# Kernel tuning notes

Measured on AMD Instinct MI355X. Metric: run time of the kernel, lower is better.

The kernel has to match this reference:

```python
import jax, jax.numpy as jnp
import numpy as np

N_NODES = 50000
N_EDGES = 600000
CH = 128


def _mlp(h, w1, b1, w2, b2):
    # Linear -> ReLU -> Linear (weights stored [in, out])
    return jax.nn.relu(h @ w1 + b1) @ w2 + b2


def setup_inputs() -> dict:
    key = jax.random.key(0)
    ks = jax.random.split(key, 12)
    def lin(k, fan_in, fan_out):
        bound = 1.0 / np.sqrt(fan_in)
        kw, kb = jax.random.split(k)
        w = jax.random.uniform(kw, (fan_in, fan_out), jnp.float32, -bound, bound)
        b = jax.random.uniform(kb, (fan_out,), jnp.float32, -bound, bound)
        return w, b
    ew1, eb1 = lin(ks[0], 3 * CH, CH)
    ew2, eb2 = lin(ks[1], CH, CH)
    nw1, nb1 = lin(ks[2], 2 * CH, CH)
    nw2, nb2 = lin(ks[3], CH, CH)
    x = jax.random.normal(ks[4], (N_NODES, CH), jnp.float32)
    edge_attr = jax.random.normal(ks[5], (N_EDGES, CH), jnp.float32)
    edge_index = jax.random.randint(ks[6], (2, N_EDGES), 0, N_NODES, jnp.int64 if jax.config.read('jax_enable_x64') else jnp.int32)
    return {"x": x, "edge_index": edge_index, "edge_attr": edge_attr,
            "ew1": ew1, "eb1": eb1, "ew2": ew2, "eb2": eb2,
            "nw1": nw1, "nb1": nb1, "nw2": nw2, "nb2": nb2}


def reference(x, edge_index, edge_attr, ew1, eb1, ew2, eb2, nw1, nb1, nw2, nb2):
    row, col = edge_index[0], edge_index[1]
    n = x.shape[0]
    # edge model: concat(source, target, edge_attr) -> MLP -> new edge_attr
    e_in = jnp.concatenate([x[row], x[col], edge_attr], axis=1)  # [E, 3*ch]
    new_edge_attr = _mlp(e_in, ew1, eb1, ew2, eb2)               # [E, ch]
    # node model: concat(x[col], new_edge_attr) -> MLP -> scatter_mean over row
    n_in = jnp.concatenate([x[col], new_edge_attr], axis=1)      # [E, 2*ch]
    msg = _mlp(n_in, nw1, nb1, nw2, nb2)                         # [E, ch]
    seg_sum = jax.ops.segment_sum(msg, row, num_segments=n)      # [N, ch]
    cnt = jax.ops.segment_sum(jnp.ones((msg.shape[0],), msg.dtype), row, num_segments=n)
    new_x = seg_sum / jnp.maximum(cnt, 1.0)[:, None]             # scatter_mean
    return new_x, new_edge_attr
```

## Files before the change

### kernel.cpp

```cpp
#include <hip/hip_runtime.h>
#include <stdint.h>

#define NN 50000
#define NE 600000
#define CH 128
#define RT 2
#define EPB 128

typedef __attribute__((ext_vector_type(8))) short short8;
typedef __attribute__((ext_vector_type(4))) float f32x4;
typedef __attribute__((ext_vector_type(4))) uint32_t u32x4;

__device__ __forceinline__ ushort f2bf(float f) {
  union { float f; uint32_t u; } v; v.f = f;
  uint32_t u = v.u;
  return (ushort)((u + 0x7FFFu + ((u >> 16) & 1u)) >> 16);
}
__device__ __forceinline__ float bf2f(uint32_t u16) {
  union { uint32_t u; float f; } t; t.u = u16 << 16; return t.f;
}
__device__ __forceinline__ uint32_t cvtpk_bf16(float a, float b) {
  uint32_t r;
  asm("v_cvt_pk_bf16_f32 %0, %1, %2" : "=v"(r) : "v"(a), "v"(b));
  return r;
}

__global__ void prep_frag_k(const float* __restrict__ ew1, const float* __restrict__ ew2,
                            const float* __restrict__ nw1, const float* __restrict__ nw2,
                            ushort* __restrict__ wB) {
  int idx = blockIdx.x * 256 + threadIdx.x;
  if (idx >= 114688) return;
  const float* src; int local;
  if (idx < 49152)      { src = ew1; local = idx; }
  else if (idx < 65536) { src = ew2; local = idx - 49152; }
  else if (idx < 98304) { src = nw1; local = idx - 65536; }
  else                  { src = nw2; local = idx - 98304; }
  int ks   = local >> 12;
  int rem  = local & 4095;
  int nt   = rem >> 9;
  int t    = rem & 511;
  int lane = t >> 3, i = t & 7;
  int k = ks * 32 + (lane >> 4) * 8 + i;
  int n = nt * 16 + (lane & 15);
  wB[idx] = f2bf(src[k * 128 + n]);
}

__global__ void convert_x_k(const float* __restrict__ x, ushort* __restrict__ xb) {
  int i = blockIdx.x * 256 + threadIdx.x;
  if (i >= NN * CH / 4) return;
  const float4 f = reinterpret_cast<const float4*>(x)[i];
  ushort4 r;
  r.x = f2bf(f.x); r.y = f2bf(f.y); r.z = f2bf(f.z); r.w = f2bf(f.w);
  reinterpret_cast<ushort4*>(xb)[i] = r;
}

__global__ void rank_k(const int* __restrict__ ei, unsigned* __restrict__ cnt,
                       unsigned* __restrict__ rank) {
  int e = blockIdx.x * 256 + threadIdx.x;
  if (e < NE) rank[e] = atomicAdd(&cnt[ei[e]], 1u);
}

__global__ void scan_k(const unsigned* __restrict__ cnt, unsigned* __restrict__ start) {
  __shared__ unsigned s[1024];
  const int CHUNK = (NN + 1023) / 1024;
  int t = threadIdx.x;
  int lo = t * CHUNK, hi = lo + CHUNK < NN ? lo + CHUNK : NN;
  unsigned sum = 0;
  for (int i = lo; i < hi; ++i) sum += cnt[i];
  s[t] = sum;
  __syncthreads();
  for (int off = 1; off < 1024; off <<= 1) {
    unsigned v = (t >= off) ? s[t - off] : 0u;
    __syncthreads();
    s[t] += v;
    __syncthreads();
  }
  unsigned run = t ? s[t - 1] : 0u;
  for (int i = lo; i < hi; ++i) { start[i] = run; run += cnt[i]; }
}

__global__ void dest_k(const int* __restrict__ ei, const unsigned* __restrict__ start,
                       const unsigned* __restrict__ rank, unsigned* __restrict__ dest) {
  int e = blockIdx.x * 256 + threadIdx.x;
  if (e < NE) dest[e] = start[ei[e]] + rank[e];
}

__device__ __forceinline__ void mm8(const ushort* Bcbuf, int lane,
                                    const short8 a[RT], f32x4 acc[RT][8]) {
#pragma unroll
  for (int nt = 0; nt < 8; ++nt) {
    short8 b = *reinterpret_cast<const short8*>(Bcbuf + nt * 512 + lane * 8);
#pragma unroll
    for (int rt = 0; rt < RT; ++rt)
      acc[rt][nt] = __builtin_amdgcn_mfma_f32_16x16x32_bf16(a[rt], b, acc[rt][nt], 0, 0, 0);
  }
}

__global__ __launch_bounds__(256, 3) void fused_k(
    const int* __restrict__ ei, const float* __restrict__ edge_attr,
    const ushort* __restrict__ wB,
    const float* __restrict__ eb1, const float* __restrict__ eb2,
    const float* __restrict__ nb1, const float* __restrict__ nb2,
    const ushort* __restrict__ xb, const unsigned* __restrict__ dest,
    ushort* __restrict__ msg, float* __restrict__ out_e)
{
  __shared__ ushort hbuf[4][RT * 16][136];
  __shared__ ushort Bc[2][4096];
  const int tid  = threadIdx.x;
  const int lane = tid & 63;
  const int widx = tid >> 6;
  const int wbase = blockIdx.x * EPB + widx * (RT * 16);
  const int l15 = lane & 15;
  const int g = lane >> 4;
  const int kg = g * 8;
  ushort (*h)[136] = hbuf[widx];

  const ushort* wsrc = wB + (size_t)tid * 16;
  short8 bt0, bt1;

#define LDB(ph) do { \
    bt0 = *reinterpret_cast<const short8*>(wsrc + (ph) * 4096); \
    bt1 = *reinterpret_cast<const short8*>(wsrc + (ph) * 4096 + 8); \
  } while (0)
#define STB(ph) do { \
    ushort* _d = &Bc[(ph) & 1][tid * 16]; \
    *reinterpret_cast<short8*>(_d) = bt0; \
    *reinterpret_cast<short8*>(_d + 8) = bt1; \
    __syncthreads(); \
  } while (0)

  int rowA[RT], colA[RT], eAc[RT];
#pragma unroll
  for (int rt = 0; rt < RT; ++rt) {
    int e = wbase + rt * 16 + l15;
    eAc[rt] = e < NE ? e : NE - 1;
    rowA[rt] = ei[eAc[rt]];
    colA[rt] = ei[NE + eAc[rt]];
  }

  const f32x4 zero4 = {0.f, 0.f, 0.f, 0.f};
  f32x4 acc[RT][8];

#pragma unroll
  for (int rt = 0; rt < RT; ++rt)
#pragma unroll
    for (int nt = 0; nt < 8; ++nt) acc[rt][nt] = zero4;

  LDB(0);
  short8 axr[4][RT], axc[4][RT];
#pragma unroll
  for (int ksl = 0; ksl < 4; ++ksl)
#pragma unroll
    for (int rt = 0; rt < RT; ++rt)
      axr[ksl][rt] = *reinterpret_cast<const short8*>(xb + rowA[rt] * CH + ksl * 32 + kg);
#pragma unroll
  for (int ksl = 0; ksl < 4; ++ksl)
#pragma unroll
    for (int rt = 0; rt < RT; ++rt)
      axc[ksl][rt] = *reinterpret_cast<const short8*>(xb + colA[rt] * CH + ksl * 32 + kg);
  STB(0);

#pragma unroll
  for (int p = 0; p < 4; ++p) {
    LDB(p + 1);
    mm8(Bc[p & 1], lane, axr[p], acc);
    STB(p + 1);
  }
#pragma unroll
  for (int p = 4; p < 8; ++p) {
    LDB(p + 1);
    mm8(Bc[p & 1], lane, axc[p - 4], acc);
    STB(p + 1);
  }
  float4 eaf[4][RT][2];
#pragma unroll
  for (int ksl = 0; ksl < 4; ++ksl)
#pragma unroll
    for (int rt = 0; rt < RT; ++rt) {
      const float* pp = edge_attr + (size_t)eAc[rt] * CH + ksl * 32 + kg;
      eaf[ksl][rt][0] = *reinterpret_cast<const float4*>(pp);
      eaf[ksl][rt][1] = *reinterpret_cast<const float4*>(pp + 4);
    }
#pragma unroll
  for (int p = 8; p < 12; ++p) {
    LDB(p + 1);
    short8 a[RT];
#pragma unroll
    for (int rt = 0; rt < RT; ++rt) {
      float4 f0 = eaf[p - 8][rt][0], f1 = eaf[p - 8][rt][1];
      union { u32x4 u; short8 s; } cv;
      cv.u = (u32x4){ cvtpk_bf16(f0.x, f0.y), cvtpk_bf16(f0.z, f0.w),
                      cvtpk_bf16(f1.x, f1.y), cvtpk_bf16(f1.z, f1.w) };
      a[rt] = cv.s;
    }
    mm8(Bc[p & 1], lane, a, acc);
    STB(p + 1);
  }
#pragma unroll
  for (int nt = 0; nt < 8; ++nt) {
    float bb = eb1[nt * 16 + l15];
#pragma unroll
    for (int rt = 0; rt < RT; ++rt)
#pragma unroll
      for (int r = 0; r < 4; r += 2) {
        float v0 = fmaxf(acc[rt][nt][r] + bb, 0.f);
        float v1 = fmaxf(acc[rt][nt][r + 1] + bb, 0.f);
        uint32_t pk = cvtpk_bf16(v0, v1);
        h[rt * 16 + g * 4 + r][nt * 16 + l15]     = (ushort)(pk & 0xffffu);
        h[rt * 16 + g * 4 + r + 1][nt * 16 + l15] = (ushort)(pk >> 16);
      }
  }

#pragma unroll
  for (int rt = 0; rt < RT; ++rt)
#pragma unroll
    for (int nt = 0; nt < 8; ++nt) acc[rt][nt] = zero4;
#pragma unroll
  for (int p = 12; p < 16; ++p) {
    LDB(p + 1);
    short8 a[RT];
#pragma unroll
    for (int rt = 0; rt < RT; ++rt)
      a[rt] = *reinterpret_cast<const short8*>(&h[rt * 16 + l15][(p - 12) * 32 + kg]);
    mm8(Bc[p & 1], lane, a, acc);
    STB(p + 1);
  }
  short8 axc2[4][RT];
#pragma unroll
  for (int ksl = 0; ksl < 4; ++ksl)
#pragma unroll
    for (int rt = 0; rt < RT; ++rt)
      axc2[ksl][rt] = *reinterpret_cast<const short8*>(xb + colA[rt] * CH + ksl * 32 + kg);
#pragma unroll
  for (int nt = 0; nt < 8; ++nt) {
    float bb = eb2[nt * 16 + l15];
#pragma unroll
    for (int rt = 0; rt < RT; ++rt) {
      float v[4];
#pragma unroll
      for (int r = 0; r < 4; ++r) {
        v[r] = acc[rt][nt][r] + bb;
        int erow = wbase + rt * 16 + g * 4 + r;
        if (erow < NE) out_e[(size_t)erow * CH + nt * 16 + l15] = v[r];
      }
#pragma unroll
      for (int r = 0; r < 4; r += 2) {
        uint32_t pk = cvtpk_bf16(v[r], v[r + 1]);
        h[rt * 16 + g * 4 + r][nt * 16 + l15]     = (ushort)(pk & 0xffffu);
        h[rt * 16 + g * 4 + r + 1][nt * 16 + l15] = (ushort)(pk >> 16);
      }
    }
  }

#pragma unroll
  for (int rt = 0; rt < RT; ++rt)
#pragma unroll
    for (int nt = 0; nt < 8; ++nt) acc[rt][nt] = zero4;
#pragma unroll
  for (int p = 16; p < 20; ++p) {
    LDB(p + 1);
    mm8(Bc[p & 1], lane, axc2[p - 16], acc);
    STB(p + 1);
  }
#pragma unroll
  for (int p = 20; p < 24; ++p) {
    LDB(p + 1);
    short8 a[RT];
#pragma unroll
    for (int rt = 0; rt < RT; ++rt)
      a[rt] = *reinterpret_cast<const short8*>(&h[rt * 16 + l15][(p - 20) * 32 + kg]);
    mm8(Bc[p & 1], lane, a, acc);
    STB(p + 1);
  }
#pragma unroll
  for (int nt = 0; nt < 8; ++nt) {
    float bb = nb1[nt * 16 + l15];
#pragma unroll
    for (int rt = 0; rt < RT; ++rt)
#pragma unroll
      for (int r = 0; r < 4; r += 2) {
        float v0 = fmaxf(acc[rt][nt][r] + bb, 0.f);
        float v1 = fmaxf(acc[rt][nt][r + 1] + bb, 0.f);
        uint32_t pk = cvtpk_bf16(v0, v1);
        h[rt * 16 + g * 4 + r][nt * 16 + l15]     = (ushort)(pk & 0xffffu);
        h[rt * 16 + g * 4 + r + 1][nt * 16 + l15] = (ushort)(pk >> 16);
      }
  }

#pragma unroll
  for (int rt = 0; rt < RT; ++rt)
#pragma unroll
    for (int nt = 0; nt < 8; ++nt) acc[rt][nt] = zero4;
#pragma unroll
  for (int p = 24; p < 27; ++p) {
    LDB(p + 1);
    short8 a[RT];
#pragma unroll
    for (int rt = 0; rt < RT; ++rt)
      a[rt] = *reinterpret_cast<const short8*>(&h[rt * 16 + l15][(p - 24) * 32 + kg]);
    mm8(Bc[p & 1], lane, a, acc);
    STB(p + 1);
  }
  {
    short8 a[RT];
#pragma unroll
    for (int rt = 0; rt < RT; ++rt)
      a[rt] = *reinterpret_cast<const short8*>(&h[rt * 16 + l15][3 * 32 + kg]);
    mm8(Bc[1], lane, a, acc);
  }
#pragma unroll
  for (int nt = 0; nt < 8; ++nt) {
    float bb = nb2[nt * 16 + l15];
#pragma unroll
    for (int rt = 0; rt < RT; ++rt)
#pragma unroll
      for (int r = 0; r < 4; r += 2) {
        uint32_t pk = cvtpk_bf16(acc[rt][nt][r] + bb, acc[rt][nt][r + 1] + bb);
        h[rt * 16 + g * 4 + r][nt * 16 + l15]     = (ushort)(pk & 0xffffu);
        h[rt * 16 + g * 4 + r + 1][nt * 16 + l15] = (ushort)(pk >> 16);
      }
  }
#pragma unroll
  for (int it = 0; it < RT * 4; ++it) {
    int row = it * 4 + g;
    int er = wbase + row;
    int col = l15 * 8;
    short8 v = *reinterpret_cast<const short8*>(&h[row][col]);
    if (er < NE) {
      unsigned dp = dest[er];
      *reinterpret_cast<short8*>(msg + (size_t)dp * CH + col) = v;
    }
  }
#undef LDB
#undef STB
}

__global__ __launch_bounds__(256) void reduce_k(const ushort* __restrict__ msg,
    const unsigned* __restrict__ cnt, const unsigned* __restrict__ start,
    float* __restrict__ out_x) {
  int w = blockIdx.x * 4 + (threadIdx.x >> 6);
  if (w >= NN) return;
  int lane = threadIdx.x & 63;
  unsigned deg = cnt[w], s = start[w];
  float a0 = 0.f, a1 = 0.f;
#pragma unroll 4
  for (unsigned j = 0; j < deg; ++j) {
    uint32_t pk = *reinterpret_cast<const uint32_t*>(msg + (size_t)(s + j) * CH + lane * 2);
    a0 += bf2f(pk & 0xffffu);
    a1 += bf2f(pk >> 16);
  }
  float inv = 1.0f / fmaxf((float)deg, 1.0f);
  float2 o; o.x = a0 * inv; o.y = a1 * inv;
  *reinterpret_cast<float2*>(out_x + (size_t)w * CH + lane * 2) = o;
}

extern "C" void kernel_launch(void* const* d_in, const int* in_sizes, int n_in,
                              void* d_out, int out_size, void* d_ws, size_t ws_size,
                              hipStream_t stream) {
  const float* x   = (const float*)d_in[0];
  const int*   ei  = (const int*)d_in[1];
  const float* ea  = (const float*)d_in[2];
  const float* ew1 = (const float*)d_in[3];
  const float* eb1 = (const float*)d_in[4];
  const float* ew2 = (const float*)d_in[5];
  const float* eb2 = (const float*)d_in[6];
  const float* nw1 = (const float*)d_in[7];
  const float* nb1 = (const float*)d_in[8];
  const float* nw2 = (const float*)d_in[9];
  const float* nb2 = (const float*)d_in[10];

  float* out_x = (float*)d_out;
  float* out_e = (float*)d_out + (size_t)NN * CH;

  char* wsb = (char*)d_ws;
  ushort*   msg    = (ushort*)wsb;
  ushort*   wB     = (ushort*)(wsb + 153600000);
  ushort*   xb     = (ushort*)(wsb + 153829376);
  unsigned* cnt    = (unsigned*)(wsb + 166629376);
  unsigned* start  = (unsigned*)(wsb + 166829376);
  unsigned* rank   = (unsigned*)(wsb + 167029376);
  unsigned* dest   = (unsigned*)(wsb + 169429376);

  hipMemsetAsync(cnt, 0, (size_t)NN * sizeof(unsigned), stream);

  prep_frag_k<<<448, 256, 0, stream>>>(ew1, ew2, nw1, nw2, wB);
  convert_x_k<<<(NN * CH / 4 + 255) / 256, 256, 0, stream>>>(x, xb);
  rank_k<<<(NE + 255) / 256, 256, 0, stream>>>(ei, cnt, rank);
  scan_k<<<1, 1024, 0, stream>>>(cnt, start);
  dest_k<<<(NE + 255) / 256, 256, 0, stream>>>(ei, start, rank, dest);

  int nblk = (NE + EPB - 1) / EPB;
  fused_k<<<nblk, 256, 0, stream>>>(ei, ea, wB, eb1, eb2, nb1, nb2, xb, dest, msg, out_e);

  reduce_k<<<(NN + 3) / 4, 256, 0, stream>>>(msg, cnt, start, out_x);
}
```

Baseline: 449.1 us.

## Use 1024-thread blocks sharing weight tiles and stream gathers just-in-time

The fused edge/node kernel now runs 16 waves per block instead of 4, so each staged weight tile in LDS is reused by four times as many edges. Each thread copies a smaller slice of the tile. The upfront gathers of x rows, x cols and edge_attr, which were held in many registers, are replaced by double-buffered per-phase prefetches. This should lower register pressure and the weight-load traffic per edge. The cost is larger per-block LDS (16 h buffers), heavier __syncthreads across 1024 threads, and less latency hiding, since each load is issued only one phase ahead.

```diff
diff --git a/kernel.cpp b/kernel.cpp
--- a/kernel.cpp
+++ b/kernel.cpp
@@ -5,7 +5,8 @@
 #define NE 600000
 #define CH 128
 #define RT 2
-#define EPB 128
+#define WAVES 16
+#define EPB (WAVES * 32)
 
 typedef __attribute__((ext_vector_type(8))) short short8;
 typedef __attribute__((ext_vector_type(4))) float f32x4;
@@ -96,7 +97,7 @@
   }
 }
 
-__global__ __launch_bounds__(256, 3) void fused_k(
+__global__ __launch_bounds__(1024, 1) void fused_k(
     const int* __restrict__ ei, const float* __restrict__ edge_attr,
     const ushort* __restrict__ wB,
     const float* __restrict__ eb1, const float* __restrict__ eb2,
@@ -104,7 +105,7 @@
     const ushort* __restrict__ xb, const unsigned* __restrict__ dest,
     ushort* __restrict__ msg, float* __restrict__ out_e)
 {
-  __shared__ ushort hbuf[4][RT * 16][136];
+  __shared__ ushort hbuf[WAVES][RT * 16][136];
   __shared__ ushort Bc[2][4096];
   const int tid  = threadIdx.x;
   const int lane = tid & 63;
@@ -115,17 +116,10 @@
   const int kg = g * 8;
   ushort (*h)[136] = hbuf[widx];
 
-  const ushort* wsrc = wB + (size_t)tid * 16;
-  short8 bt0, bt1;
-
-#define LDB(ph) do { \
-    bt0 = *reinterpret_cast<const short8*>(wsrc + (ph) * 4096); \
-    bt1 = *reinterpret_cast<const short8*>(wsrc + (ph) * 4096 + 8); \
-  } while (0)
+  ushort4 bt;
+#define LDB(ph) do { bt = *reinterpret_cast<const ushort4*>(wB + (size_t)(ph) * 4096 + tid * 4); } while (0)
 #define STB(ph) do { \
-    ushort* _d = &Bc[(ph) & 1][tid * 16]; \
-    *reinterpret_cast<short8*>(_d) = bt0; \
-    *reinterpret_cast<short8*>(_d + 8) = bt1; \
+    *reinterpret_cast<ushort4*>(&Bc[(ph) & 1][tid * 4]) = bt; \
     __syncthreads(); \
   } while (0)
 
@@ -146,48 +140,52 @@
 #pragma unroll
     for (int nt = 0; nt < 8; ++nt) acc[rt][nt] = zero4;
 
+  short8 ax[2][RT];
+  float4 ea2[2][RT][2];
+
   LDB(0);
-  short8 axr[4][RT], axc[4][RT];
-#pragma unroll
-  for (int ksl = 0; ksl < 4; ++ksl)
-#pragma unroll
-    for (int rt = 0; rt < RT; ++rt)
-      axr[ksl][rt] = *reinterpret_cast<const short8*>(xb + rowA[rt] * CH + ksl * 32 + kg);
-#pragma unroll
-  for (int ksl = 0; ksl < 4; ++ksl)
-#pragma unroll
-    for (int rt = 0; rt < RT; ++rt)
-      axc[ksl][rt] = *reinterpret_cast<const short8*>(xb + colA[rt] * CH + ksl * 32 + kg);
+#pragma unroll
+  for (int rt = 0; rt < RT; ++rt)
+    ax[0][rt] = *reinterpret_cast<const short8*>(xb + rowA[rt] * CH + kg);
   STB(0);
 
 #pragma unroll
-  for (int p = 0; p < 4; ++p) {
-    LDB(p + 1);
-    mm8(Bc[p & 1], lane, axr[p], acc);
-    STB(p + 1);
-  }
-#pragma unroll
-  for (int p = 4; p < 8; ++p) {
-    LDB(p + 1);
-    mm8(Bc[p & 1], lane, axc[p - 4], acc);
-    STB(p + 1);
-  }
-  float4 eaf[4][RT][2];
-#pragma unroll
-  for (int ksl = 0; ksl < 4; ++ksl)
+  for (int p = 0; p < 8; ++p) {
+    LDB(p + 1);
+    if (p + 1 < 4) {
+#pragma unroll
+      for (int rt = 0; rt < RT; ++rt)
+        ax[(p + 1) & 1][rt] = *reinterpret_cast<const short8*>(xb + rowA[rt] * CH + (p + 1) * 32 + kg);
+    } else if (p + 1 < 8) {
+#pragma unroll
+      for (int rt = 0; rt < RT; ++rt)
+        ax[(p + 1) & 1][rt] = *reinterpret_cast<const short8*>(xb + colA[rt] * CH + (p + 1 - 4) * 32 + kg);
+    } else {
+#pragma unroll
+      for (int rt = 0; rt < RT; ++rt) {
+        const float* pp = edge_attr + (size_t)eAc[rt] * CH + kg;
+        ea2[0][rt][0] = *reinterpret_cast<const float4*>(pp);
+        ea2[0][rt][1] = *reinterpret_cast<const float4*>(pp + 4);
+      }
+    }
+    mm8(Bc[p & 1], lane, ax[p & 1], acc);
+    STB(p + 1);
+  }
+#pragma unroll
+  for (int p = 8; p < 12; ++p) {
+    LDB(p + 1);
+    if (p < 11) {
+#pragma unroll
+      for (int rt = 0; rt < RT; ++rt) {
+        const float* pp = edge_attr + (size_t)eAc[rt] * CH + (p - 7) * 32 + kg;
+        ea2[(p + 1) & 1][rt][0] = *reinterpret_cast<const float4*>(pp);
+        ea2[(p + 1) & 1][rt][1] = *reinterpret_cast<const float4*>(pp + 4);
+      }
+    }
+    short8 a[RT];
 #pragma unroll
     for (int rt = 0; rt < RT; ++rt) {
-      const float* pp = edge_attr + (size_t)eAc[rt] * CH + ksl * 32 + kg;
-      eaf[ksl][rt][0] = *reinterpret_cast<const float4*>(pp);
-      eaf[ksl][rt][1] = *reinterpret_cast<const float4*>(pp + 4);
-    }
-#pragma unroll
-  for (int p = 8; p < 12; ++p) {
-    LDB(p + 1);
-    short8 a[RT];
-#pragma unroll
-    for (int rt = 0; rt < RT; ++rt) {
-      float4 f0 = eaf[p - 8][rt][0], f1 = eaf[p - 8][rt][1];
+      float4 f0 = ea2[p & 1][rt][0], f1 = ea2[p & 1][rt][1];
       union { u32x4 u; short8 s; } cv;
       cv.u = (u32x4){ cvtpk_bf16(f0.x, f0.y), cvtpk_bf16(f0.z, f0.w),
                       cvtpk_bf16(f1.x, f1.y), cvtpk_bf16(f1.z, f1.w) };
@@ -211,6 +209,7 @@
       }
   }
 
+  short8 axc2[4][RT];
 #pragma unroll
   for (int rt = 0; rt < RT; ++rt)
 #pragma unroll
@@ -218,6 +217,9 @@
 #pragma unroll
   for (int p = 12; p < 16; ++p) {
     LDB(p + 1);
+#pragma unroll
+    for (int rt = 0; rt < RT; ++rt)
+      axc2[p - 12][rt] = *reinterpret_cast<const short8*>(xb + colA[rt] * CH + (p - 12) * 32 + kg);
     short8 a[RT];
 #pragma unroll
     for (int rt = 0; rt < RT; ++rt)
@@ -225,12 +227,6 @@
     mm8(Bc[p & 1], lane, a, acc);
     STB(p + 1);
   }
-  short8 axc2[4][RT];
-#pragma unroll
-  for (int ksl = 0; ksl < 4; ++ksl)
-#pragma unroll
-    for (int rt = 0; rt < RT; ++rt)
-      axc2[ksl][rt] = *reinterpret_cast<const short8*>(xb + colA[rt] * CH + ksl * 32 + kg);
 #pragma unroll
   for (int nt = 0; nt < 8; ++nt) {
     float bb = eb2[nt * 16 + l15];
@@ -390,7 +386,7 @@
   dest_k<<<(NE + 255) / 256, 256, 0, stream>>>(ei, start, rank, dest);
 
   int nblk = (NE + EPB - 1) / EPB;
-  fused_k<<<nblk, 256, 0, stream>>>(ei, ea, wB, eb1, eb2, nb1, nb2, xb, dest, msg, out_e);
+  fused_k<<<nblk, 1024, 0, stream>>>(ei, ea, wB, eb1, eb2, nb1, nb2, xb, dest, msg, out_e);
 
   reduce_k<<<(NN + 3) / 4, 256, 0, stream>>>(msg, cnt, start, out_x);
 }
```

After: 580.0 us. 29.2% more time.

## Stage weight slices two at a time with quad LDS buffer and fewer barriers

Applied to the files above, without the earlier changes.

Restructures the weight-streaming pipeline so each barrier covers two 32-wide K slices, using a 4-slot LDS ring and two register sets of prefetched weight data. Barrier count drops by about half. Other changes: the second x[col] gather is removed by reusing axc, edge_attr is converted to bf16 at load time, dest indices are prefetched early, and MFMA blocks run at raised wave priority. It costs more registers and LDS, and occupancy is lowered from 3 to 2 blocks per CU.

```diff
diff --git a/kernel.cpp b/kernel.cpp
--- a/kernel.cpp
+++ b/kernel.cpp
@@ -96,7 +96,7 @@
   }
 }
 
-__global__ __launch_bounds__(256, 3) void fused_k(
+__global__ __launch_bounds__(256, 2) void fused_k(
     const int* __restrict__ ei, const float* __restrict__ edge_attr,
     const ushort* __restrict__ wB,
     const float* __restrict__ eb1, const float* __restrict__ eb2,
@@ -105,7 +105,7 @@
     ushort* __restrict__ msg, float* __restrict__ out_e)
 {
   __shared__ ushort hbuf[4][RT * 16][136];
-  __shared__ ushort Bc[2][4096];
+  __shared__ ushort Bc[4][4096];
   const int tid  = threadIdx.x;
   const int lane = tid & 63;
   const int widx = tid >> 6;
@@ -115,19 +115,40 @@
   const int kg = g * 8;
   ushort (*h)[136] = hbuf[widx];
 
-  const ushort* wsrc = wB + (size_t)tid * 16;
-  short8 bt0, bt1;
-
-#define LDB(ph) do { \
-    bt0 = *reinterpret_cast<const short8*>(wsrc + (ph) * 4096); \
-    bt1 = *reinterpret_cast<const short8*>(wsrc + (ph) * 4096 + 8); \
+  short8 bt[2][4];
+
+#define LDB2(set, ph) do { \
+    const ushort* _s = wB + (size_t)(ph) * 4096 + tid * 16; \
+    bt[set][0] = *reinterpret_cast<const short8*>(_s); \
+    bt[set][1] = *reinterpret_cast<const short8*>(_s + 8); \
+    bt[set][2] = *reinterpret_cast<const short8*>(_s + 4096); \
+    bt[set][3] = *reinterpret_cast<const short8*>(_s + 4096 + 8); \
   } while (0)
-#define STB(ph) do { \
-    ushort* _d = &Bc[(ph) & 1][tid * 16]; \
-    *reinterpret_cast<short8*>(_d) = bt0; \
-    *reinterpret_cast<short8*>(_d + 8) = bt1; \
+#define STB2(set, ph) do { \
+    ushort* _d0 = &Bc[(ph) & 3][tid * 16]; \
+    ushort* _d1 = &Bc[((ph) + 1) & 3][tid * 16]; \
+    *reinterpret_cast<short8*>(_d0)     = bt[set][0]; \
+    *reinterpret_cast<short8*>(_d0 + 8) = bt[set][1]; \
+    *reinterpret_cast<short8*>(_d1)     = bt[set][2]; \
+    *reinterpret_cast<short8*>(_d1 + 8) = bt[set][3]; \
+  } while (0)
+#define STEP(s, A0, A1, DO_LDB, DO_STB) do { \
     __syncthreads(); \
+    __builtin_amdgcn_s_setprio(1); \
+    mm8(Bc[(2 * (s)) & 3], lane, A0, acc); \
+    mm8(Bc[(2 * (s) + 1) & 3], lane, A1, acc); \
+    __builtin_amdgcn_s_setprio(0); \
+    if (DO_LDB) LDB2((s) & 1, 2 * (s) + 4); \
+    if (DO_STB) STB2(((s) + 1) & 1, 2 * (s) + 2); \
   } while (0)
+#define LDH(dst, ksl) do { \
+    _Pragma("unroll") \
+    for (int _rt = 0; _rt < RT; ++_rt) \
+      dst[_rt] = *reinterpret_cast<const short8*>(&h[_rt * 16 + l15][(ksl) * 32 + kg]); \
+  } while (0)
+
+  LDB2(0, 0);
+  LDB2(1, 2);
 
   int rowA[RT], colA[RT], eAc[RT];
 #pragma unroll
@@ -137,65 +158,51 @@
     rowA[rt] = ei[eAc[rt]];
     colA[rt] = ei[NE + eAc[rt]];
   }
-
-  const f32x4 zero4 = {0.f, 0.f, 0.f, 0.f};
-  f32x4 acc[RT][8];
-
-#pragma unroll
-  for (int rt = 0; rt < RT; ++rt)
-#pragma unroll
-    for (int nt = 0; nt < 8; ++nt) acc[rt][nt] = zero4;
-
-  LDB(0);
   short8 axr[4][RT], axc[4][RT];
 #pragma unroll
   for (int ksl = 0; ksl < 4; ++ksl)
 #pragma unroll
-    for (int rt = 0; rt < RT; ++rt)
+    for (int rt = 0; rt < RT; ++rt) {
       axr[ksl][rt] = *reinterpret_cast<const short8*>(xb + rowA[rt] * CH + ksl * 32 + kg);
-#pragma unroll
-  for (int ksl = 0; ksl < 4; ++ksl)
-#pragma unroll
-    for (int rt = 0; rt < RT; ++rt)
       axc[ksl][rt] = *reinterpret_cast<const short8*>(xb + colA[rt] * CH + ksl * 32 + kg);
-  STB(0);
-
-#pragma unroll
-  for (int p = 0; p < 4; ++p) {
-    LDB(p + 1);
-    mm8(Bc[p & 1], lane, axr[p], acc);
-    STB(p + 1);
-  }
-#pragma unroll
-  for (int p = 4; p < 8; ++p) {
-    LDB(p + 1);
-    mm8(Bc[p & 1], lane, axc[p - 4], acc);
-    STB(p + 1);
-  }
-  float4 eaf[4][RT][2];
+    }
+  short8 eab[4][RT];
 #pragma unroll
   for (int ksl = 0; ksl < 4; ++ksl)
 #pragma unroll
     for (int rt = 0; rt < RT; ++rt) {
       const float* pp = edge_attr + (size_t)eAc[rt] * CH + ksl * 32 + kg;
-      eaf[ksl][rt][0] = *reinterpret_cast<const float4*>(pp);
-      eaf[ksl][rt][1] = *reinterpret_cast<const float4*>(pp + 4);
-    }
-#pragma unroll
-  for (int p = 8; p < 12; ++p) {
-    LDB(p + 1);
-    short8 a[RT];
-#pragma unroll
-    for (int rt = 0; rt < RT; ++rt) {
-      float4 f0 = eaf[p - 8][rt][0], f1 = eaf[p - 8][rt][1];
+      float4 f0 = *reinterpret_cast<const float4*>(pp);
+      float4 f1 = *reinterpret_cast<const float4*>(pp + 4);
       union { u32x4 u; short8 s; } cv;
       cv.u = (u32x4){ cvtpk_bf16(f0.x, f0.y), cvtpk_bf16(f0.z, f0.w),
                       cvtpk_bf16(f1.x, f1.y), cvtpk_bf16(f1.z, f1.w) };
-      a[rt] = cv.s;
+      eab[ksl][rt] = cv.s;
     }
-    mm8(Bc[p & 1], lane, a, acc);
-    STB(p + 1);
-  }
+  unsigned dp[RT * 4];
+#pragma unroll
+  for (int it = 0; it < RT * 4; ++it) {
+    int er = wbase + it * 4 + g;
+    dp[it] = dest[er < NE ? er : NE - 1];
+  }
+
+  STB2(0, 0);
+
+  const f32x4 zero4 = {0.f, 0.f, 0.f, 0.f};
+  f32x4 acc[RT][8];
+  short8 ha0[RT], ha1[RT];
+
+#pragma unroll
+  for (int rt = 0; rt < RT; ++rt)
+#pragma unroll
+    for (int nt = 0; nt < 8; ++nt) acc[rt][nt] = zero4;
+
+  STEP(0, axr[0], axr[1], 1, 1);
+  STEP(1, axr[2], axr[3], 1, 1);
+  STEP(2, axc[0], axc[1], 1, 1);
+  STEP(3, axc[2], axc[3], 1, 1);
+  STEP(4, eab[0], eab[1], 1, 1);
+  STEP(5, eab[2], eab[3], 1, 1);
 #pragma unroll
   for (int nt = 0; nt < 8; ++nt) {
     float bb = eb1[nt * 16 + l15];
@@ -215,22 +222,10 @@
   for (int rt = 0; rt < RT; ++rt)
 #pragma unroll
     for (int nt = 0; nt < 8; ++nt) acc[rt][nt] = zero4;
-#pragma unroll
-  for (int p = 12; p < 16; ++p) {
-    LDB(p + 1);
-    short8 a[RT];
-#pragma unroll
-    for (int rt = 0; rt < RT; ++rt)
-      a[rt] = *reinterpret_cast<const short8*>(&h[rt * 16 + l15][(p - 12) * 32 + kg]);
-    mm8(Bc[p & 1], lane, a, acc);
-    STB(p + 1);
-  }
-  short8 axc2[4][RT];
-#pragma unroll
-  for (int ksl = 0; ksl < 4; ++ksl)
-#pragma unroll
-    for (int rt = 0; rt < RT; ++rt)
-      axc2[ksl][rt] = *reinterpret_cast<const short8*>(xb + colA[rt] * CH + ksl * 32 + kg);
+  LDH(ha0, 0); LDH(ha1, 1);
+  STEP(6, ha0, ha1, 1, 1);
+  LDH(ha0, 2); LDH(ha1, 3);
+  STEP(7, ha0, ha1, 1, 1);
 #pragma unroll
   for (int nt = 0; nt < 8; ++nt) {
     float bb = eb2[nt * 16 + l15];
@@ -256,22 +251,12 @@
   for (int rt = 0; rt < RT; ++rt)
 #pragma unroll
     for (int nt = 0; nt < 8; ++nt) acc[rt][nt] = zero4;
-#pragma unroll
-  for (int p = 16; p < 20; ++p) {
-    LDB(p + 1);
-    mm8(Bc[p & 1], lane, axc2[p - 16], acc);
-    STB(p + 1);
-  }
-#pragma unroll
-  for (int p = 20; p < 24; ++p) {
-    LDB(p + 1);
-    short8 a[RT];
-#pragma unroll
-    for (int rt = 0; rt < RT; ++rt)
-      a[rt] = *reinterpret_cast<const short8*>(&h[rt * 16 + l15][(p - 20) * 32 + kg]);
-    mm8(Bc[p & 1], lane, a, acc);
-    STB(p + 1);
-  }
+  STEP(8, axc[0], axc[1], 1, 1);
+  STEP(9, axc[2], axc[3], 1, 1);
+  LDH(ha0, 0); LDH(ha1, 1);
+  STEP(10, ha0, ha1, 1, 1);
+  LDH(ha0, 2); LDH(ha1, 3);
+  STEP(11, ha0, ha1, 1, 1);
 #pragma unroll
   for (int nt = 0; nt < 8; ++nt) {
     float bb = nb1[nt * 16 + l15];
@@ -291,23 +276,10 @@
   for (int rt = 0; rt < RT; ++rt)
 #pragma unroll
     for (int nt = 0; nt < 8; ++nt) acc[rt][nt] = zero4;
-#pragma unroll
-  for (int p = 24; p < 27; ++p) {
-    LDB(p + 1);
-    short8 a[RT];
-#pragma unroll
-    for (int rt = 0; rt < RT; ++rt)
-      a[rt] = *reinterpret_cast<const short8*>(&h[rt * 16 + l15][(p - 24) * 32 + kg]);
-    mm8(Bc[p & 1], lane, a, acc);
-    STB(p + 1);
-  }
-  {
-    short8 a[RT];
-#pragma unroll
-    for (int rt = 0; rt < RT; ++rt)
-      a[rt] = *reinterpret_cast<const short8*>(&h[rt * 16 + l15][3 * 32 + kg]);
-    mm8(Bc[1], lane, a, acc);
-  }
+  LDH(ha0, 0); LDH(ha1, 1);
+  STEP(12, ha0, ha1, 0, 1);
+  LDH(ha0, 2); LDH(ha1, 3);
+  STEP(13, ha0, ha1, 0, 0);
 #pragma unroll
   for (int nt = 0; nt < 8; ++nt) {
     float bb = nb2[nt * 16 + l15];
@@ -326,13 +298,13 @@
     int er = wbase + row;
     int col = l15 * 8;
     short8 v = *reinterpret_cast<const short8*>(&h[row][col]);
-    if (er < NE) {
-      unsigned dp = dest[er];
-      *reinterpret_cast<short8*>(msg + (size_t)dp * CH + col) = v;
-    }
-  }
-#undef LDB
-#undef STB
+    if (er < NE)
+      *reinterpret_cast<short8*>(msg + (size_t)dp[it] * CH + col) = v;
+  }
+#undef LDB2
+#undef STB2
+#undef STEP
+#undef LDH
 }
 
 __global__ __launch_bounds__(256) void reduce_k(const ushort* __restrict__ msg,
```

New measurement: 431.8 us. 1.04x faster.
